# Kernel tuning notes

Hardware: AMD Instinct MI355X
Metric: run time of the kernel (lower is better)

The kernel has to match this reference:

```python
import jax, jax.numpy as jnp
import numpy as np

NU, NM, D, E = 100000, 20000, 128, 1000000


def _seg_mean(feats, idx, n):
    # scatter-mean: zero for nodes with no incoming edges (PyG semantics)
    s = jax.ops.segment_sum(feats, idx, num_segments=n)
    c = jax.ops.segment_sum(jnp.ones((idx.shape[0], 1), feats.dtype), idx, num_segments=n)
    return s / jnp.maximum(c, 1.0)


def _hetero_sage(xu, xm, e_src, e_dst, Wl_um, Wr_um, b_um, Wl_mu, Wr_mu, b_mu):
    # ('user','rates','movie'): aggregate user features at movies
    agg_m = _seg_mean(xu[e_src], e_dst, xm.shape[0])          # [Nm, D]
    out_m = agg_m @ Wl_um + b_um + xm @ Wr_um                  # [Nm, H]
    # ('movie','rev_rates','user'): aggregate movie features at users
    agg_u = _seg_mean(xm[e_dst], e_src, xu.shape[0])          # [Nu, D]
    out_u = agg_u @ Wl_mu + b_mu + xu @ Wr_mu                  # [Nu, H]
    return out_u, out_m


def setup_inputs() -> dict:
    key = jax.random.key(0)
    ks = jax.random.split(key, 20)
    glorot = lambda k: (jax.random.normal(k, (D, D), jnp.float32) / np.sqrt(D)).astype(jnp.float32)
    inp = {
        "x_user": jax.random.normal(ks[0], (NU, D), jnp.float32),
        "x_movie": jax.random.normal(ks[1], (NM, D), jnp.float32),
        "edge_src": jax.random.randint(ks[2], (E,), 0, NU),
        "edge_dst": jax.random.randint(ks[3], (E,), 0, NM),
    }
    names = ["Wl1_um", "Wr1_um", "Wl1_mu", "Wr1_mu", "Wl2_um", "Wr2_um", "Wl2_mu", "Wr2_mu"]
    for i, n in enumerate(names):
        inp[n] = glorot(ks[4 + i])
    inp["b1_um"] = jnp.zeros((D,), jnp.float32)
    inp["b1_mu"] = jnp.zeros((D,), jnp.float32)
    inp["b2_um"] = jnp.zeros((D,), jnp.float32)
    inp["b2_mu"] = jnp.zeros((D,), jnp.float32)
    return inp


def reference(x_user, x_movie, Wl1_um, Wr1_um, Wl1_mu, Wr1_mu, Wl2_um, Wr2_um, Wl2_mu, Wr2_mu, b1_um, b1_mu, b2_um, b2_mu, edge_src, edge_dst):
    # layer 1 + relu (dropout = identity in eval) + residual
    h1_u, h1_m = _hetero_sage(x_user, x_movie, edge_src, edge_dst,
                              Wl1_um, Wr1_um, b1_um, Wl1_mu, Wr1_mu, b1_mu)
    r_u = x_user + jax.nn.relu(h1_u)
    r_m = x_movie + jax.nn.relu(h1_m)
    # layer 2 (dropout = identity in eval)
    out_u, out_m = _hetero_sage(r_u, r_m, edge_src, edge_dst,
                                Wl2_um, Wr2_um, b2_um, Wl2_mu, Wr2_mu, b2_mu)
    return out_u, out_m
```

## Files before the change

kernel.cpp:

```cpp
#include <hip/hip_runtime.h>
#include <stdint.h>

typedef unsigned short u16;
typedef unsigned int u32;
typedef __attribute__((ext_vector_type(8))) short short8;
typedef __attribute__((ext_vector_type(4))) float f32x4;
typedef __attribute__((ext_vector_type(4))) u32 u32x4;

__device__ __forceinline__ u16 f2bf(float f) {
    u32 x = __float_as_uint(f);
    u32 r = x + 0x7FFFu + ((x >> 16) & 1u);
    return (u16)(r >> 16);
}
__device__ __forceinline__ u32 pack2bf(float a, float b) {
    return (u32)f2bf(a) | ((u32)f2bf(b) << 16);
}
__device__ __forceinline__ float bflo(u32 w) { return __uint_as_float(w << 16); }
__device__ __forceinline__ float bfhi(u32 w) { return __uint_as_float(w & 0xFFFF0000u); }

struct WPtrs {
    const float* wl[4];
    const float* wr[4];
    u16* wout[4];
};

__global__ __launch_bounds__(256)
void prep_kernel(const int* __restrict__ src, const int* __restrict__ dst,
                 int* __restrict__ cnt, int* __restrict__ ranku,
                 int* __restrict__ rankm, int E, int nu, int nm,
                 const float* __restrict__ xu, const float* __restrict__ xm,
                 u32* __restrict__ xub, u32* __restrict__ xmb,
                 int eg4, int cg, WPtrs wp) {
    const int bid = blockIdx.x;
    const int tid = threadIdx.x;
    if (bid < eg4) {
        const int e0 = bid * 1024 + tid;
        int sv[4], dv[4];
        bool ok[4];
#pragma unroll
        for (int k = 0; k < 4; ++k) {
            int e = e0 + k * 256;
            ok[k] = (e < E);
            if (ok[k]) { sv[k] = src[e]; dv[k] = dst[e]; }
        }
#pragma unroll
        for (int k = 0; k < 4; ++k) {
            int e = e0 + k * 256;
            if (ok[k]) {
                if ((unsigned)sv[k] < (unsigned)nu &&
                    (unsigned)dv[k] < (unsigned)nm) {
                    ranku[e] = atomicAdd(&cnt[sv[k]], 1);
                    rankm[e] = atomicAdd(&cnt[nu + dv[k]], 1);
                } else {
                    ranku[e] = -1;
                }
            }
        }
    } else if (bid < eg4 + cg) {
        const int id = (bid - eg4) * 1024 + tid * 4;
        const int nuc = nu * 64;
        const int tot = nuc + nm * 64;
        if (id < tot) {
            const float* fin;
            u32* fout;
            int rel;
            if (id < nuc) { fin = xu; fout = xub; rel = id; }
            else          { fin = xm; fout = xmb; rel = id - nuc; }
            float4 p0 = ((const float4*)fin)[(rel >> 1)];
            float4 p1 = ((const float4*)fin)[(rel >> 1) + 1];
            u32x4 o = { pack2bf(p0.x, p0.y), pack2bf(p0.z, p0.w),
                        pack2bf(p1.x, p1.y), pack2bf(p1.z, p1.w) };
            *(u32x4*)(fout + rel) = o;
        }
    } else {
        const int unit = (bid - eg4 - cg) * 4 + (tid >> 6);
        if (unit < 256) {
            const int stack = unit >> 6, r = unit & 63, t = r >> 3, s = r & 7;
            const int lane = tid & 63;
            const float* Wl = wp.wl[stack];
            const float* Wr = wp.wr[stack];
            u16* outw = wp.wout[stack];
            const int n = t * 16 + (lane & 15);
            const int k0 = s * 32 + (lane >> 4) * 8;
            u16 v[8];
#pragma unroll
            for (int j = 0; j < 8; ++j) {
                int k = k0 + j;
                float f = (k < 128) ? Wl[k * 128 + n] : Wr[(k - 128) * 128 + n];
                v[j] = f2bf(f);
            }
            *(short8*)(outw + ((size_t)(t * 8 + s) * 64 + lane) * 8) = *(short8*)v;
        }
    }
}

__global__ __launch_bounds__(256)
void scan_partial(const int* __restrict__ cnt, int* __restrict__ bsum, int n) {
    __shared__ int s[256];
    const int tid = threadIdx.x;
    int base = blockIdx.x * 4096 + tid * 16;
    int sum = 0;
#pragma unroll
    for (int k = 0; k < 16; ++k) {
        int i = base + k;
        if (i < n) sum += cnt[i];
    }
    s[tid] = sum;
    __syncthreads();
    for (int d = 128; d > 0; d >>= 1) {
        if (tid < d) s[tid] += s[tid + d];
        __syncthreads();
    }
    if (tid == 0) bsum[blockIdx.x] = s[0];
}

__global__ __launch_bounds__(256)
void scan_apply(const int* __restrict__ cnt, const int* __restrict__ bsum,
                int* __restrict__ off, int n, int nb) {
    __shared__ int s[256];
    __shared__ int sb[64];
    __shared__ int pfx;
    const int tid = threadIdx.x;
    int base = blockIdx.x * 4096 + tid * 16;
    int v[16];
    int sum = 0;
#pragma unroll
    for (int k = 0; k < 16; ++k) {
        int i = base + k;
        v[k] = (i < n) ? cnt[i] : 0;
        sum += v[k];
    }
    s[tid] = sum;
    if (tid < 64) sb[tid] = (tid < nb) ? bsum[tid] : 0;
    __syncthreads();
    for (int d = 1; d < 256; d <<= 1) {
        int t = (tid >= d) ? s[tid - d] : 0;
        __syncthreads();
        s[tid] += t;
        __syncthreads();
    }
    if (tid == 0) {
        int p = 0;
        for (int b2 = 0; b2 < (int)blockIdx.x; ++b2) p += sb[b2];
        pfx = p;
        if ((int)blockIdx.x == nb - 1) off[n] = p + s[255];
    }
    __syncthreads();
    int run = pfx + s[tid] - sum;
#pragma unroll
    for (int k = 0; k < 16; ++k) {
        int i = base + k;
        if (i < n) off[i] = run;
        run += v[k];
    }
}

__global__ __launch_bounds__(256)
void fill_pos(const int* __restrict__ src, const int* __restrict__ dst,
              const int* __restrict__ ranku, const int* __restrict__ rankm,
              const int* __restrict__ off, int* __restrict__ nbr,
              int E, int nu) {
    const int e0 = blockIdx.x * 1024 + threadIdx.x;
    int sv[4], dv[4], ru[4], rm[4];
#pragma unroll
    for (int k = 0; k < 4; ++k) {
        int e = e0 + k * 256;
        ru[k] = -1;
        if (e < E) {
            ru[k] = ranku[e];
            sv[k] = src[e]; dv[k] = dst[e]; rm[k] = rankm[e];
        }
    }
#pragma unroll
    for (int k = 0; k < 4; ++k) {
        if (ru[k] >= 0) {
            nbr[off[sv[k]] + ru[k]] = dv[k];
            nbr[off[nu + dv[k]] + rm[k]] = sv[k];
        }
    }
}

template <int L1>
__device__ __forceinline__ void fused_body(
    const u32* __restrict__ featb, const float* __restrict__ xf,
    const u32* __restrict__ xb, const int* __restrict__ off,
    const int* __restrict__ nbr, const u16* __restrict__ wt,
    const float* __restrict__ bias, void* __restrict__ outp, int N, int blk) {
    __shared__ u32 sVb[16][132];
    const int tid = threadIdx.x;
    const int lane = tid & 63;
    const int wave = tid >> 6;
    const int base = blk * 16;
    const int q = lane >> 4;
    const int cl = lane & 15;

#pragma unroll
    for (int gg = 0; gg < 2; ++gg) {
        const int i = wave * 8 + gg * 4 + q;
        const int n = base + i;
        int b = 0, e2 = 0;
        if (n < N) { b = off[n]; e2 = off[n + 1]; }
        const int deg = e2 - b;
        float a0 = 0.f, a1 = 0.f, a2 = 0.f, a3 = 0.f;
        float a4 = 0.f, a5 = 0.f, a6 = 0.f, a7 = 0.f;
        for (int j = 0; j < deg; j += 4) {
            const int p = b + j;
            const int p1 = (p + 1 < e2) ? p + 1 : e2 - 1;
            const int p2 = (p + 2 < e2) ? p + 2 : e2 - 1;
            const int p3 = (p + 3 < e2) ? p + 3 : e2 - 1;
            const float m1 = (p + 1 < e2) ? 1.f : 0.f;
            const float m2 = (p + 2 < e2) ? 1.f : 0.f;
            const float m3 = (p + 3 < e2) ? 1.f : 0.f;
            const int g0 = nbr[p];
            const int g1 = nbr[p1];
            const int g2 = nbr[p2];
            const int g3 = nbr[p3];
            u32x4 v0 = *(const u32x4*)(featb + (size_t)g0 * 64 + cl * 4);
            u32x4 v1 = *(const u32x4*)(featb + (size_t)g1 * 64 + cl * 4);
            u32x4 v2 = *(const u32x4*)(featb + (size_t)g2 * 64 + cl * 4);
            u32x4 v3 = *(const u32x4*)(featb + (size_t)g3 * 64 + cl * 4);
            a0 += bflo(v0.x); a1 += bfhi(v0.x); a2 += bflo(v0.y); a3 += bfhi(v0.y);
            a4 += bflo(v0.z); a5 += bfhi(v0.z); a6 += bflo(v0.w); a7 += bfhi(v0.w);
            a0 = fmaf(bflo(v1.x), m1, a0); a1 = fmaf(bfhi(v1.x), m1, a1);
            a2 = fmaf(bflo(v1.y), m1, a2); a3 = fmaf(bfhi(v1.y), m1, a3);
            a4 = fmaf(bflo(v1.z), m1, a4); a5 = fmaf(bfhi(v1.z), m1, a5);
            a6 = fmaf(bflo(v1.w), m1, a6); a7 = fmaf(bfhi(v1.w), m1, a7);
            a0 = fmaf(bflo(v2.x), m2, a0); a1 = fmaf(bfhi(v2.x), m2, a1);
            a2 = fmaf(bflo(v2.y), m2, a2); a3 = fmaf(bfhi(v2.y), m2, a3);
            a4 = fmaf(bflo(v2.z), m2, a4); a5 = fmaf(bfhi(v2.z), m2, a5);
            a6 = fmaf(bflo(v2.w), m2, a6); a7 = fmaf(bfhi(v2.w), m2, a7);
            a0 = fmaf(bflo(v3.x), m3, a0); a1 = fmaf(bfhi(v3.x), m3, a1);
            a2 = fmaf(bflo(v3.y), m3, a2); a3 = fmaf(bfhi(v3.y), m3, a3);
            a4 = fmaf(bflo(v3.z), m3, a4); a5 = fmaf(bfhi(v3.z), m3, a5);
            a6 = fmaf(bflo(v3.w), m3, a6); a7 = fmaf(bfhi(v3.w), m3, a7);
        }
        const float inv = 1.0f / (float)(deg > 1 ? deg : 1);
        u32x4 o = { pack2bf(a0 * inv, a1 * inv), pack2bf(a2 * inv, a3 * inv),
                    pack2bf(a4 * inv, a5 * inv), pack2bf(a6 * inv, a7 * inv) };
        *(u32x4*)&sVb[i][cl * 4] = o;
    }
    for (int c = 0; c < 8; ++c) {
        const int i = wave * 8 + c;
        const int n = base + i;
        if (n < N) {
            if (L1) {
                const float2 xv = ((const float2*)xf)[(size_t)n * 64 + lane];
                sVb[i][64 + lane] = pack2bf(xv.x, xv.y);
            } else {
                sVb[i][64 + lane] = xb[(size_t)n * 64 + lane];
            }
        } else {
            sVb[i][64 + lane] = 0u;
        }
    }
    __syncthreads();

    const int t0 = wave * 4;
    const u16* sVbu = (const u16*)sVb;
    const short8* wtp = (const short8*)wt;

    f32x4 acc0 = {0.f, 0.f, 0.f, 0.f};
    f32x4 acc1 = {0.f, 0.f, 0.f, 0.f};
    f32x4 acc2 = {0.f, 0.f, 0.f, 0.f};
    f32x4 acc3 = {0.f, 0.f, 0.f, 0.f};
#pragma unroll
    for (int s = 0; s < 8; ++s) {
        short8 a = *(const short8*)(sVbu + (size_t)cl * 264 + s * 32 + q * 8);
        short8 b0 = wtp[(size_t)((t0 + 0) * 8 + s) * 64 + lane];
        short8 b1 = wtp[(size_t)((t0 + 1) * 8 + s) * 64 + lane];
        short8 b2 = wtp[(size_t)((t0 + 2) * 8 + s) * 64 + lane];
        short8 b3 = wtp[(size_t)((t0 + 3) * 8 + s) * 64 + lane];
        acc0 = __builtin_amdgcn_mfma_f32_16x16x32_bf16(a, b0, acc0, 0, 0, 0);
        acc1 = __builtin_amdgcn_mfma_f32_16x16x32_bf16(a, b1, acc1, 0, 0, 0);
        acc2 = __builtin_amdgcn_mfma_f32_16x16x32_bf16(a, b2, acc2, 0, 0, 0);
        acc3 = __builtin_amdgcn_mfma_f32_16x16x32_bf16(a, b3, acc3, 0, 0, 0);
    }

#pragma unroll
    for (int tt = 0; tt < 4; ++tt) {
        const f32x4& cc = tt == 0 ? acc0 : tt == 1 ? acc1 : tt == 2 ? acc2 : acc3;
        const int nn = (t0 + tt) * 16 + cl;
        const float bj = bias[nn];
#pragma unroll
        for (int r = 0; r < 4; ++r) {
            const int m = q * 4 + r;
            const int node = base + m;
            if (node < N) {
                float h = cc[r] + bj;
                if (L1) {
                    u16* ob = (u16*)outp;
                    float x0 = xf[(size_t)node * 128 + nn];
                    ob[(size_t)node * 128 + nn] = f2bf(x0 + fmaxf(h, 0.f));
                } else {
                    float* o = (float*)outp;
                    o[(size_t)node * 128 + nn] = h;
                }
            }
        }
    }
}

__global__ __launch_bounds__(128, 8)
void fused_l1(const u32* __restrict__ featb, const float* __restrict__ xf,
              const int* __restrict__ off, const int* __restrict__ nbr,
              const u16* __restrict__ wt, const float* __restrict__ bias,
              void* __restrict__ outp, int N) {
    fused_body<1>(featb, xf, nullptr, off, nbr, wt, bias, outp, N, blockIdx.x);
}

__global__ __launch_bounds__(128, 8)
void fused_l2_dual(const u32* __restrict__ Abf, const u32* __restrict__ rmb,
                   const int* __restrict__ off, const int* __restrict__ nbr,
                   const u16* __restrict__ wtm, const u16* __restrict__ wtu,
                   const float* __restrict__ bm, const float* __restrict__ bu,
                   float* __restrict__ outm, float* __restrict__ outu,
                   int nm, int nu, int gm) {
    if ((int)blockIdx.x < gm)
        fused_body<0>(Abf, nullptr, rmb, off + nu, nbr, wtm, bm, outm, nm,
                      blockIdx.x);
    else
        fused_body<0>(rmb, nullptr, Abf, off, nbr, wtu, bu, outu, nu,
                      blockIdx.x - gm);
}

extern "C" void kernel_launch(void* const* d_in, const int* in_sizes, int n_in,
                              void* d_out, int out_size, void* d_ws, size_t ws_size,
                              hipStream_t stream) {
    const int nu = in_sizes[0] / 128;
    const int nm = in_sizes[1] / 128;
    const int E = in_sizes[2];

    const float* xu = (const float*)d_in[0];
    const float* xm = (const float*)d_in[1];
    const int* esrc = (const int*)d_in[2];
    const int* edst = (const int*)d_in[3];
    const float* Wl1_um = (const float*)d_in[4];
    const float* Wr1_um = (const float*)d_in[5];
    const float* Wl1_mu = (const float*)d_in[6];
    const float* Wr1_mu = (const float*)d_in[7];
    const float* Wl2_um = (const float*)d_in[8];
    const float* Wr2_um = (const float*)d_in[9];
    const float* Wl2_mu = (const float*)d_in[10];
    const float* Wr2_mu = (const float*)d_in[11];
    const float* b1_um = (const float*)d_in[12];
    const float* b1_mu = (const float*)d_in[13];
    const float* b2_um = (const float*)d_in[14];
    const float* b2_mu = (const float*)d_in[15];

    float* out_u = (float*)d_out;
    float* out_m = out_u + (size_t)nu * 128;

    const int ntot = nu + nm;
    const int NB = (ntot + 4095) / 4096;
    int* cnt = (int*)d_ws;
    int* off = cnt + ntot;
    int* bsum = off + ntot + 1;
    int* ranku = bsum + ((NB + 15) & ~15);
    int* rankm = ranku + E;
    int* nbr = rankm + E;
    size_t int_bytes = (size_t)((nbr + 2 * (size_t)E) - (int*)d_ws) * 4;
    size_t wt_off = (int_bytes + 63) & ~(size_t)63;
    u16* wt1_um = (u16*)((char*)d_ws + wt_off);
    u16* wt1_mu = wt1_um + 32768;
    u16* wt2_um = wt1_mu + 32768;
    u16* wt2_mu = wt2_um + 32768;
    u32* Abf = (u32*)((char*)d_ws + wt_off + 4 * 65536);
    u32* xmb = Abf + (size_t)nu * 64;
    u32* rmb = xmb + (size_t)nm * 64;

    const int eg4 = (E + 1023) / 1024;
    const int cg = ((nu + nm) * 64 + 1023) / 1024;

    WPtrs wp;
    wp.wl[0] = Wl1_um; wp.wr[0] = Wr1_um; wp.wout[0] = wt1_um;
    wp.wl[1] = Wl1_mu; wp.wr[1] = Wr1_mu; wp.wout[1] = wt1_mu;
    wp.wl[2] = Wl2_um; wp.wr[2] = Wr2_um; wp.wout[2] = wt2_um;
    wp.wl[3] = Wl2_mu; wp.wr[3] = Wr2_mu; wp.wout[3] = wt2_mu;

    hipMemsetAsync(cnt, 0, (size_t)ntot * 4, stream);
    prep_kernel<<<eg4 + cg + 64, 256, 0, stream>>>(
        esrc, edst, cnt, ranku, rankm, E, nu, nm, xu, xm, Abf, xmb, eg4, cg, wp);
    scan_partial<<<NB, 256, 0, stream>>>(cnt, bsum, ntot);
    scan_apply<<<NB, 256, 0, stream>>>(cnt, bsum, off, ntot, NB);
    fill_pos<<<eg4, 256, 0, stream>>>(esrc, edst, ranku, rankm, off, nbr, E, nu);

    const int gm = (nm + 15) / 16;
    const int gu = (nu + 15) / 16;

    fused_l1<<<gm, 128, 0, stream>>>(Abf, xm, off + nu, nbr, wt1_um, b1_um,
                                     rmb, nm);
    fused_l1<<<gu, 128, 0, stream>>>(xmb, xu, off, nbr, wt1_mu, b1_mu,
                                     Abf, nu);

    fused_l2_dual<<<gm + gu, 128, 0, stream>>>(
        Abf, rmb, off, nbr, wt2_um, wt2_mu, b2_um, b2_mu, out_m, out_u,
        nm, nu, gm);
}
```

Measured before the change: 480.5 us.

## Split CSR build per direction, pad atomic counters, overlap user fill with movie layer

Builds the movie-side CSR first, with its own scan and fill. The user-side degree counting then runs inside the movie fill kernel, and the user neighbour fill runs alongside the layer-1 movie aggregation in one combined launch. Counters are spaced eight ints apart to cut atomic contention and false sharing between adjacent nodes. This adds kernel launches and uses more counter memory, and it relies on the movie layer-1 blocks not reading the user half of the neighbour array while it is being written.

Result: slower. 500.2 us (+4.1%).

```diff
diff --git a/kernel.cpp b/kernel.cpp
--- a/kernel.cpp
+++ b/kernel.cpp
@@ -7,6 +7,8 @@
 typedef __attribute__((ext_vector_type(4))) float f32x4;
 typedef __attribute__((ext_vector_type(4))) u32 u32x4;
 
+#define CSTR 8
+
 __device__ __forceinline__ u16 f2bf(float f) {
     u32 x = __float_as_uint(f);
     u32 r = x + 0x7FFFu + ((x >> 16) & 1u);
@@ -25,15 +27,15 @@
 };
 
 __global__ __launch_bounds__(256)
-void prep_kernel(const int* __restrict__ src, const int* __restrict__ dst,
-                 int* __restrict__ cnt, int* __restrict__ ranku,
-                 int* __restrict__ rankm, int E, int nu, int nm,
-                 const float* __restrict__ xu, const float* __restrict__ xm,
-                 u32* __restrict__ xub, u32* __restrict__ xmb,
-                 int eg4, int cg, WPtrs wp) {
+void prep_a(const int* __restrict__ src, const int* __restrict__ dst,
+            int* __restrict__ cnt, int* __restrict__ rankm,
+            int E, int nu, int nm,
+            const float* __restrict__ xu, const float* __restrict__ xm,
+            u32* __restrict__ xub, u32* __restrict__ xmb,
+            int egH, int cg, WPtrs wp) {
     const int bid = blockIdx.x;
     const int tid = threadIdx.x;
-    if (bid < eg4) {
+    if (bid < egH) {
         const int e0 = bid * 1024 + tid;
         int sv[4], dv[4];
         bool ok[4];
@@ -49,15 +51,14 @@
             if (ok[k]) {
                 if ((unsigned)sv[k] < (unsigned)nu &&
                     (unsigned)dv[k] < (unsigned)nm) {
-                    ranku[e] = atomicAdd(&cnt[sv[k]], 1);
-                    rankm[e] = atomicAdd(&cnt[nu + dv[k]], 1);
+                    rankm[e] = atomicAdd(&cnt[(size_t)(nu + dv[k]) * CSTR], 1);
                 } else {
-                    ranku[e] = -1;
+                    rankm[e] = -1;
                 }
             }
         }
-    } else if (bid < eg4 + cg) {
-        const int id = (bid - eg4) * 1024 + tid * 4;
+    } else if (bid < egH + cg) {
+        const int id = (bid - egH) * 1024 + tid * 4;
         const int nuc = nu * 64;
         const int tot = nuc + nm * 64;
         if (id < tot) {
@@ -73,7 +74,7 @@
             *(u32x4*)(fout + rel) = o;
         }
     } else {
-        const int unit = (bid - eg4 - cg) * 4 + (tid >> 6);
+        const int unit = (bid - egH - cg) * 4 + (tid >> 6);
         if (unit < 256) {
             const int stack = unit >> 6, r = unit & 63, t = r >> 3, s = r & 7;
             const int lane = tid & 63;
@@ -95,6 +96,54 @@
 }
 
 __global__ __launch_bounds__(256)
+void prep_b(const int* __restrict__ src, const int* __restrict__ dst,
+            int* __restrict__ cnt, int* __restrict__ ranku,
+            const int* __restrict__ rankm, const int* __restrict__ off,
+            int* __restrict__ nbr, int E, int nu, int nm, int egF) {
+    const int bid = blockIdx.x;
+    const int tid = threadIdx.x;
+    if (bid < egF) {
+        const int e0 = bid * 1024 + tid;
+        int sv[4], dv[4], rm[4];
+#pragma unroll
+        for (int k = 0; k < 4; ++k) {
+            int e = e0 + k * 256;
+            rm[k] = -1;
+            if (e < E) {
+                rm[k] = rankm[e];
+                sv[k] = src[e]; dv[k] = dst[e];
+            }
+        }
+#pragma unroll
+        for (int k = 0; k < 4; ++k) {
+            if (rm[k] >= 0) nbr[off[nu + dv[k]] + rm[k]] = sv[k];
+        }
+    } else {
+        const int e0 = (bid - egF) * 1024 + tid;
+        int sv[4], dv[4];
+        bool ok[4];
+#pragma unroll
+        for (int k = 0; k < 4; ++k) {
+            int e = e0 + k * 256;
+            ok[k] = (e < E);
+            if (ok[k]) { sv[k] = src[e]; dv[k] = dst[e]; }
+        }
+#pragma unroll
+        for (int k = 0; k < 4; ++k) {
+            int e = e0 + k * 256;
+            if (ok[k]) {
+                if ((unsigned)sv[k] < (unsigned)nu &&
+                    (unsigned)dv[k] < (unsigned)nm) {
+                    ranku[e] = atomicAdd(&cnt[(size_t)sv[k] * CSTR], 1);
+                } else {
+                    ranku[e] = -1;
+                }
+            }
+        }
+    }
+}
+
+__global__ __launch_bounds__(256)
 void scan_partial(const int* __restrict__ cnt, int* __restrict__ bsum, int n) {
     __shared__ int s[256];
     const int tid = threadIdx.x;
@@ -103,7 +152,7 @@
 #pragma unroll
     for (int k = 0; k < 16; ++k) {
         int i = base + k;
-        if (i < n) sum += cnt[i];
+        if (i < n) sum += cnt[(size_t)i * CSTR];
     }
     s[tid] = sum;
     __syncthreads();
@@ -116,7 +165,7 @@
 
 __global__ __launch_bounds__(256)
 void scan_apply(const int* __restrict__ cnt, const int* __restrict__ bsum,
-                int* __restrict__ off, int n, int nb) {
+                int* __restrict__ off, int n, int nb, int addbase) {
     __shared__ int s[256];
     __shared__ int sb[64];
     __shared__ int pfx;
@@ -127,7 +176,7 @@
 #pragma unroll
     for (int k = 0; k < 16; ++k) {
         int i = base + k;
-        v[k] = (i < n) ? cnt[i] : 0;
+        v[k] = (i < n) ? cnt[(size_t)i * CSTR] : 0;
         sum += v[k];
     }
     s[tid] = sum;
@@ -143,40 +192,15 @@
         int p = 0;
         for (int b2 = 0; b2 < (int)blockIdx.x; ++b2) p += sb[b2];
         pfx = p;
-        if ((int)blockIdx.x == nb - 1) off[n] = p + s[255];
+        if ((int)blockIdx.x == nb - 1) off[n] = addbase + p + s[255];
     }
     __syncthreads();
-    int run = pfx + s[tid] - sum;
+    int run = addbase + pfx + s[tid] - sum;
 #pragma unroll
     for (int k = 0; k < 16; ++k) {
         int i = base + k;
         if (i < n) off[i] = run;
         run += v[k];
-    }
-}
-
-__global__ __launch_bounds__(256)
-void fill_pos(const int* __restrict__ src, const int* __restrict__ dst,
-              const int* __restrict__ ranku, const int* __restrict__ rankm,
-              const int* __restrict__ off, int* __restrict__ nbr,
-              int E, int nu) {
-    const int e0 = blockIdx.x * 1024 + threadIdx.x;
-    int sv[4], dv[4], ru[4], rm[4];
-#pragma unroll
-    for (int k = 0; k < 4; ++k) {
-        int e = e0 + k * 256;
-        ru[k] = -1;
-        if (e < E) {
-            ru[k] = ranku[e];
-            sv[k] = src[e]; dv[k] = dst[e]; rm[k] = rankm[e];
-        }
-    }
-#pragma unroll
-    for (int k = 0; k < 4; ++k) {
-        if (ru[k] >= 0) {
-            nbr[off[sv[k]] + ru[k]] = dv[k];
-            nbr[off[nu + dv[k]] + rm[k]] = sv[k];
-        }
     }
 }
 
@@ -301,6 +325,36 @@
 }
 
 __global__ __launch_bounds__(128, 8)
+void l1movie_fillu(const u32* __restrict__ Abf, const float* __restrict__ xm,
+                   const int* __restrict__ off, const int* __restrict__ nbr_r,
+                   const u16* __restrict__ wt, const float* __restrict__ bias,
+                   void* __restrict__ outp, int nm, int nu, int gm,
+                   const int* __restrict__ src, const int* __restrict__ dst,
+                   const int* __restrict__ ranku, int* __restrict__ nbr_w,
+                   int E) {
+    if ((int)blockIdx.x < gm) {
+        fused_body<1>(Abf, xm, nullptr, off + nu, nbr_r, wt, bias, outp, nm,
+                      blockIdx.x);
+    } else {
+        const int e0 = ((int)blockIdx.x - gm) * 1024 + (int)threadIdx.x;
+        int sv[8], dv[8], ru[8];
+#pragma unroll
+        for (int k = 0; k < 8; ++k) {
+            int e = e0 + k * 128;
+            ru[k] = -1;
+            if (e < E) {
+                ru[k] = ranku[e];
+                sv[k] = src[e]; dv[k] = dst[e];
+            }
+        }
+#pragma unroll
+        for (int k = 0; k < 8; ++k) {
+            if (ru[k] >= 0) nbr_w[off[sv[k]] + ru[k]] = dv[k];
+        }
+    }
+}
+
+__global__ __launch_bounds__(128, 8)
 void fused_l1(const u32* __restrict__ featb, const float* __restrict__ xf,
               const int* __restrict__ off, const int* __restrict__ nbr,
               const u16* __restrict__ wt, const float* __restrict__ bias,
@@ -351,11 +405,10 @@
     float* out_m = out_u + (size_t)nu * 128;
 
     const int ntot = nu + nm;
-    const int NB = (ntot + 4095) / 4096;
     int* cnt = (int*)d_ws;
-    int* off = cnt + ntot;
+    int* off = cnt + (size_t)ntot * CSTR;
     int* bsum = off + ntot + 1;
-    int* ranku = bsum + ((NB + 15) & ~15);
+    int* ranku = bsum + 64;
     int* rankm = ranku + E;
     int* nbr = rankm + E;
     size_t int_bytes = (size_t)((nbr + 2 * (size_t)E) - (int*)d_ws) * 4;
@@ -368,8 +421,11 @@
     u32* xmb = Abf + (size_t)nu * 64;
     u32* rmb = xmb + (size_t)nm * 64;
 
-    const int eg4 = (E + 1023) / 1024;
-    const int cg = ((nu + nm) * 64 + 1023) / 1024;
+    const int egH = (E + 1023) / 1024;
+    const int egF = (E + 1023) / 1024;
+    const int cg = (ntot * 64 + 1023) / 1024;
+    const int NBm = (nm + 4095) / 4096;
+    const int NBu = (nu + 4095) / 4096;
 
     WPtrs wp;
     wp.wl[0] = Wl1_um; wp.wr[0] = Wr1_um; wp.wout[0] = wt1_um;
@@ -377,21 +433,24 @@
     wp.wl[2] = Wl2_um; wp.wr[2] = Wr2_um; wp.wout[2] = wt2_um;
     wp.wl[3] = Wl2_mu; wp.wr[3] = Wr2_mu; wp.wout[3] = wt2_mu;
 
-    hipMemsetAsync(cnt, 0, (size_t)ntot * 4, stream);
-    prep_kernel<<<eg4 + cg + 64, 256, 0, stream>>>(
-        esrc, edst, cnt, ranku, rankm, E, nu, nm, xu, xm, Abf, xmb, eg4, cg, wp);
-    scan_partial<<<NB, 256, 0, stream>>>(cnt, bsum, ntot);
-    scan_apply<<<NB, 256, 0, stream>>>(cnt, bsum, off, ntot, NB);
-    fill_pos<<<eg4, 256, 0, stream>>>(esrc, edst, ranku, rankm, off, nbr, E, nu);
-
     const int gm = (nm + 15) / 16;
     const int gu = (nu + 15) / 16;
 
-    fused_l1<<<gm, 128, 0, stream>>>(Abf, xm, off + nu, nbr, wt1_um, b1_um,
-                                     rmb, nm);
+    hipMemsetAsync(cnt, 0, (size_t)ntot * CSTR * 4, stream);
+    prep_a<<<egH + cg + 64, 256, 0, stream>>>(
+        esrc, edst, cnt, rankm, E, nu, nm, xu, xm, Abf, xmb, egH, cg, wp);
+    scan_partial<<<NBm, 256, 0, stream>>>(cnt + (size_t)nu * CSTR, bsum, nm);
+    scan_apply<<<NBm, 256, 0, stream>>>(cnt + (size_t)nu * CSTR, bsum,
+                                        off + nu, nm, NBm, E);
+    prep_b<<<2 * egF, 256, 0, stream>>>(esrc, edst, cnt, ranku, rankm, off,
+                                        nbr, E, nu, nm, egF);
+    scan_partial<<<NBu, 256, 0, stream>>>(cnt, bsum, nu);
+    scan_apply<<<NBu, 256, 0, stream>>>(cnt, bsum, off, nu, NBu, 0);
+    l1movie_fillu<<<gm + egF, 128, 0, stream>>>(
+        Abf, xm, off, nbr, wt1_um, b1_um, rmb, nm, nu, gm,
+        esrc, edst, ranku, nbr, E);
     fused_l1<<<gu, 128, 0, stream>>>(xmb, xu, off, nbr, wt1_mu, b1_mu,
                                      Abf, nu);
-
     fused_l2_dual<<<gm + gu, 128, 0, stream>>>(
         Abf, rmb, off, nbr, wt2_um, wt2_mu, b2_um, b2_mu, out_m, out_u,
         nm, nu, gm);
```
